# Kernel tuning notes

Hardware: AMD Instinct MI355X
Metric: run time of the kernel (lower is better)

Reference implementation:

```python
import jax, jax.numpy as jnp
import numpy as np

N = 100000      # nodes
F_IN = 512      # input features
HID = 256       # hidden
C = 50          # classes
E = 1_600_000   # edges
K = 10          # APPNP iterations
ALPHA = 1.0     # teleport prob (as hard-coded in source: APPNP(10, 1))


def setup_inputs() -> dict:
    key = jax.random.key(0)
    k1, k2, k3, k4, k5, k6 = jax.random.split(key, 6)
    x = jax.random.normal(k1, (N, F_IN), dtype=jnp.float32)
    edge_index = jax.random.randint(k2, (2, E), 0, N, dtype=jnp.int32)
    # Linear params (torch nn.Linear default init scale ~ 1/sqrt(fan_in))
    W1 = jax.random.uniform(k3, (F_IN, HID), jnp.float32, -1.0, 1.0) / np.sqrt(F_IN)
    b1 = jax.random.uniform(k4, (HID,), jnp.float32, -1.0, 1.0) / np.sqrt(F_IN)
    W2 = jax.random.uniform(k5, (HID, C), jnp.float32, -1.0, 1.0) / np.sqrt(HID)
    b2 = jax.random.uniform(k6, (C,), jnp.float32, -1.0, 1.0) / np.sqrt(HID)
    return {"x": x, "edge_index": edge_index, "W1": W1, "b1": b1, "W2": W2, "b2": b2}


def _appnp(h, edge_index):
    # gcn_norm with self-loops: A_hat = D^{-1/2} (A + I) D^{-1/2}
    loops = jnp.arange(N, dtype=edge_index.dtype)
    src = jnp.concatenate([edge_index[0], loops])  # message sources
    dst = jnp.concatenate([edge_index[1], loops])  # aggregation targets
    deg = jax.ops.segment_sum(jnp.ones_like(dst, dtype=h.dtype), dst, num_segments=N)
    dinv = jnp.where(deg > 0, jax.lax.rsqrt(deg), 0.0)
    norm = (dinv[src] * dinv[dst])[:, None]  # [E+N, 1]

    def step(z, _):
        agg = jax.ops.segment_sum(norm * z[src], dst, num_segments=N)  # [N, C]
        z = (1.0 - ALPHA) * agg + ALPHA * h
        return z, None

    z, _ = jax.lax.scan(step, h, None, length=K)
    return z


def reference(x, edge_index, W1, b1, W2, b2):
    # eval mode: dropout is identity
    h = jax.nn.relu(x @ W1 + b1)   # [N, HID]
    h = h @ W2 + b2                # [N, C]
    z = _appnp(h, edge_index)      # K-step personalized-pagerank propagation
    return jax.nn.log_softmax(z, axis=1)
```

## Files before the change

kernel.cpp:

```cpp
#include <hip/hip_runtime.h>
#include <cstdint>
#include <cstddef>

#define NROWS 100000
#define FIN 512
#define HIDDEN 256
#define NCLS 50

typedef __attribute__((ext_vector_type(8))) short s16x8;
typedef __attribute__((ext_vector_type(4))) float f32x4;

__device__ __forceinline__ unsigned short f2bf(float f) {
  unsigned int u = __float_as_uint(f);
  u += 0x7fffu + ((u >> 16) & 1u);
  return (unsigned short)(u >> 16);
}

__device__ __forceinline__ unsigned int cvt_pk_bf16(float lo, float hi) {
  unsigned int r;
  asm("v_cvt_pk_bf16_f32 %0, %1, %2" : "=v"(r) : "v"(lo), "v"(hi));
  return r;
}

__device__ __forceinline__ void gload_lds16(const void* g, void* l) {
  __builtin_amdgcn_global_load_lds(
      (const __attribute__((address_space(1))) void*)g,
      (__attribute__((address_space(3))) void*)l, 16, 0, 0);
}

__device__ __forceinline__ f32x4 mfma_bf16(s16x8 a, s16x8 b, f32x4 c) {
  return __builtin_amdgcn_mfma_f32_16x16x32_bf16(a, b, c, 0, 0, 0);
}

__global__ __launch_bounds__(256) void prep_kernel(
    const float* __restrict__ W1, const float* __restrict__ W2,
    unsigned short* __restrict__ w1t, unsigned short* __restrict__ w2t) {
  __shared__ float tile[64][65];
  const int b = blockIdx.x, t = threadIdx.x;
  if (b < 32) {
    const int k0 = (b >> 2) * 64, n0 = (b & 3) * 64;
    const int rq = t >> 6, col = t & 63;
#pragma unroll
    for (int i = 0; i < 16; ++i) {
      int row = i * 4 + rq;
      tile[row][col] = W1[(size_t)(k0 + row) * HIDDEN + n0 + col];
    }
    __syncthreads();
#pragma unroll
    for (int i = 0; i < 16; ++i) {
      int n = i * 4 + rq;
      w1t[(size_t)(n0 + n) * FIN + k0 + col] = f2bf(tile[col][n]);
    }
  } else {
    const int b2i = b - 32;
#pragma unroll
    for (int i = 0; i < 16; ++i) {
      int idx = t + i * 256;
      int c = idx >> 6;
      int k = b2i * 64 + (idx & 63);
      float v = (c < NCLS) ? W2[(size_t)k * NCLS + c] : 0.0f;
      w2t[(size_t)c * HIDDEN + k] = f2bf(v);
    }
  }
}

__global__ __launch_bounds__(512, 4) void fused_kernel(
    const float* __restrict__ x, const unsigned short* __restrict__ w1t,
    const unsigned short* __restrict__ w2t, const float* __restrict__ b1,
    const float* __restrict__ b2, float* __restrict__ out) {
  __shared__ char smem[65536];
  float* const Abase = (float*)smem;
  unsigned short* const Bbase = (unsigned short*)(smem + 32768);

  const int t = threadIdx.x;
  const int lane = t & 63, wid = t >> 6;
  const int q = lane & 15, half = lane >> 4;
  const int wr = wid >> 1, wc = wid & 1;
  const int bm = blockIdx.x;

  auto stage_A = [&](float* buf, int k0) {
#pragma unroll
    for (int i = 0; i < 2; ++i) {
      int c = t + i * 512;
      int row = c >> 3, s = c & 7;
      int grow = bm * 128 + row;
      if (grow > NROWS - 1) grow = NROWS - 1;
      gload_lds16(x + (size_t)grow * FIN + k0 + ((s ^ (row & 7)) << 2),
                  buf + c * 4);
    }
  };
  auto stage_B = [&](unsigned short* buf, int k0) {
#pragma unroll
    for (int i = 0; i < 2; ++i) {
      int c = t + i * 512;
      int col = c >> 2, s = c & 3;
      gload_lds16(w1t + (size_t)col * FIN + k0 + ((s ^ ((col >> 2) & 3)) << 3),
                  buf + c * 8);
    }
  };

  f32x4 acc[2][8];
  const f32x4 z4 = {0.f, 0.f, 0.f, 0.f};
#pragma unroll
  for (int m = 0; m < 2; ++m)
#pragma unroll
    for (int n = 0; n < 8; ++n) acc[m][n] = z4;

  auto kstep_compute = [&](int cur) {
    float* Ac = Abase + cur * 4096;
    unsigned short* Bc = Bbase + cur * 8192;
    s16x8 af[2];
#pragma unroll
    for (int m = 0; m < 2; ++m) {
      const int row = wr * 32 + m * 16 + q;
      const int cb = row * 8;
      f32x4 lo = *(const f32x4*)(Ac + (cb + ((half * 2) ^ (q & 7))) * 4);
      f32x4 hi = *(const f32x4*)(Ac + (cb + ((half * 2 + 1) ^ (q & 7))) * 4);
      union { unsigned int u[4]; s16x8 v; } cvu;
      cvu.u[0] = cvt_pk_bf16(lo[0], lo[1]);
      cvu.u[1] = cvt_pk_bf16(lo[2], lo[3]);
      cvu.u[2] = cvt_pk_bf16(hi[0], hi[1]);
      cvu.u[3] = cvt_pk_bf16(hi[2], hi[3]);
      af[m] = cvu.v;
    }
#pragma unroll
    for (int n = 0; n < 8; ++n) {
      const int col = wc * 128 + n * 16 + q;
      s16x8 bf = *(const s16x8*)(Bc + col * 32 + ((half ^ ((q >> 2) & 3)) << 3));
      acc[0][n] = mfma_bf16(af[0], bf, acc[0][n]);
      acc[1][n] = mfma_bf16(af[1], bf, acc[1][n]);
    }
  };

  stage_A(Abase, 0);
  stage_B(Bbase, 0);
  asm volatile("s_waitcnt vmcnt(0)" ::: "memory");
  __builtin_amdgcn_s_barrier();
  __builtin_amdgcn_sched_barrier(0);

  for (int ks = 0; ks < 15; ++ks) {
    const int cur = ks & 1;
    stage_A(Abase + (cur ^ 1) * 4096, (ks + 1) * 32);
    stage_B(Bbase + (cur ^ 1) * 8192, (ks + 1) * 32);
    asm volatile("s_waitcnt vmcnt(4)" ::: "memory");
    __builtin_amdgcn_s_barrier();
    __builtin_amdgcn_sched_barrier(0);
    kstep_compute(cur);
    __builtin_amdgcn_s_barrier();
    __builtin_amdgcn_sched_barrier(0);
  }
  asm volatile("s_waitcnt vmcnt(0)" ::: "memory");
  __builtin_amdgcn_s_barrier();
  __builtin_amdgcn_sched_barrier(0);
  kstep_compute(1);
  __syncthreads();

  unsigned short* const hls = (unsigned short*)smem;
  unsigned short* const wls = Bbase;
  const int p_of_wave = wid >> 2;

#pragma unroll
  for (int i = 0; i < 4; ++i) {
    int c = t + i * 512;
    int row = c >> 5, s = c & 31;
    gload_lds16(w2t + (size_t)row * HIDDEN + ((s ^ (row & 7)) << 3), wls + c * 8);
  }

  auto write_h = [&]() {
#pragma unroll
    for (int n = 0; n < 8; ++n) {
      const int col = wc * 128 + n * 16 + q;
      const float bias = b1[col];
      const int chs = col & 7;
#pragma unroll
      for (int m = 0; m < 2; ++m) {
        const int rl0 = (wr & 1) * 32 + m * 16 + half * 4;
#pragma unroll
        for (int r = 0; r < 4; ++r) {
          const int rl = rl0 + r;
          float v = fmaxf(acc[m][n][r] + bias, 0.0f);
          const int ch = (col >> 3) ^ (rl & 7);
          hls[rl * 256 + ch * 8 + chs] = f2bf(v);
        }
      }
    }
  };

  auto gemm2_pass = [&](int p) {
    f32x4 acc2[4];
#pragma unroll
    for (int n = 0; n < 4; ++n) acc2[n] = z4;
    const int arl = (wid & 3) * 16 + q;
#pragma unroll
    for (int ks = 0; ks < HIDDEN; ks += 32) {
      const int g = (ks >> 3) + half;
      s16x8 a2 = *(const s16x8*)(hls + arl * 256 + ((g ^ (arl & 7)) << 3));
#pragma unroll
      for (int n = 0; n < 4; ++n) {
        const int c = n * 16 + q;
        s16x8 b2f = *(const s16x8*)(wls + c * 256 + ((g ^ (c & 7)) << 3));
        acc2[n] = mfma_bf16(a2, b2f, acc2[n]);
      }
    }
    float bias2[4];
#pragma unroll
    for (int n = 0; n < 4; ++n) {
      const int c = n * 16 + q;
      bias2[n] = (c < NCLS) ? b2[c] : 0.0f;
    }
#pragma unroll
    for (int r = 0; r < 4; ++r) {
      float vals[4];
      float mx = -1e30f;
#pragma unroll
      for (int n = 0; n < 4; ++n) {
        const int c = n * 16 + q;
        float v = acc2[n][r] + bias2[n];
        vals[n] = v;
        if (c < NCLS) mx = fmaxf(mx, v);
      }
      for (int off = 8; off >= 1; off >>= 1)
        mx = fmaxf(mx, __shfl_xor(mx, off, 64));
      float s = 0.f;
#pragma unroll
      for (int n = 0; n < 4; ++n) {
        const int c = n * 16 + q;
        if (c < NCLS) s += __expf(vals[n] - mx);
      }
      for (int off = 8; off >= 1; off >>= 1) s += __shfl_xor(s, off, 64);
      const float lz = __logf(s);
      const int rowg = bm * 128 + p * 64 + (wid & 3) * 16 + half * 4 + r;
      if (rowg < NROWS) {
#pragma unroll
        for (int n = 0; n < 4; ++n) {
          const int c = n * 16 + q;
          if (c < NCLS) out[(size_t)rowg * NCLS + c] = vals[n] - mx - lz;
        }
      }
    }
  };

  if (p_of_wave == 0) write_h();
  __syncthreads();
  if (p_of_wave == 0) gemm2_pass(0);
  __syncthreads();
  if (p_of_wave == 1) write_h();
  __syncthreads();
  if (p_of_wave == 1) gemm2_pass(1);
}

extern "C" void kernel_launch(void* const* d_in, const int* in_sizes, int n_in,
                              void* d_out, int out_size, void* d_ws, size_t ws_size,
                              hipStream_t stream) {
  const float* x  = (const float*)d_in[0];
  const float* W1 = (const float*)d_in[2];
  const float* b1 = (const float*)d_in[3];
  const float* W2 = (const float*)d_in[4];
  const float* b2 = (const float*)d_in[5];
  float* out = (float*)d_out;

  char* ws = (char*)d_ws;
  unsigned short* w1t = (unsigned short*)(ws);
  unsigned short* w2t = (unsigned short*)(ws + 262144);

  prep_kernel<<<36, 256, 0, stream>>>(W1, W2, w1t, w2t);
  fused_kernel<<<(NROWS + 127) / 128, 512, 0, stream>>>(x, w1t, w2t, b1, b2, out);
}
```

Measured before the change: 69.27 us.

## Shrink block tile to 64 rows and stage x as bf16 via registers

Reworks the fused MLP kernel to use 256-thread blocks over 64-row tiles. fp32 x is loaded into registers, converted to bf16 once, and stored in LDS, replacing fp32 staging with a conversion on every fragment read. LDS use drops from 64KB to 40KB, and the second GEMM now reads W2 fragments directly from global memory in a single pass. The aim is higher occupancy and less LDS traffic, at the cost of more W1 re-reads per row and register-staged loads.

```diff
diff --git a/kernel.cpp b/kernel.cpp
--- a/kernel.cpp
+++ b/kernel.cpp
@@ -64,189 +64,184 @@
   }
 }
 
-__global__ __launch_bounds__(512, 4) void fused_kernel(
+__global__ __launch_bounds__(256, 4) void fused_kernel(
     const float* __restrict__ x, const unsigned short* __restrict__ w1t,
     const unsigned short* __restrict__ w2t, const float* __restrict__ b1,
     const float* __restrict__ b2, float* __restrict__ out) {
-  __shared__ char smem[65536];
-  float* const Abase = (float*)smem;
-  unsigned short* const Bbase = (unsigned short*)(smem + 32768);
+  __shared__ char smem[40960];
+  unsigned short* const Abuf = (unsigned short*)smem;
+  unsigned short* const Bbuf = (unsigned short*)(smem + 8192);
 
   const int t = threadIdx.x;
   const int lane = t & 63, wid = t >> 6;
   const int q = lane & 15, half = lane >> 4;
-  const int wr = wid >> 1, wc = wid & 1;
   const int bm = blockIdx.x;
 
-  auto stage_A = [&](float* buf, int k0) {
-#pragma unroll
-    for (int i = 0; i < 2; ++i) {
-      int c = t + i * 512;
-      int row = c >> 3, s = c & 7;
-      int grow = bm * 128 + row;
-      if (grow > NROWS - 1) grow = NROWS - 1;
-      gload_lds16(x + (size_t)grow * FIN + k0 + ((s ^ (row & 7)) << 2),
-                  buf + c * 4);
-    }
-  };
-  auto stage_B = [&](unsigned short* buf, int k0) {
-#pragma unroll
-    for (int i = 0; i < 2; ++i) {
-      int c = t + i * 512;
-      int col = c >> 2, s = c & 3;
-      gload_lds16(w1t + (size_t)col * FIN + k0 + ((s ^ ((col >> 2) & 3)) << 3),
-                  buf + c * 8);
-    }
-  };
-
-  f32x4 acc[2][8];
+  {
+    int growA = bm * 64 + (t >> 2);
+    if (growA > NROWS - 1) growA = NROWS - 1;
+  }
+  int growA = bm * 64 + (t >> 2);
+  if (growA > NROWS - 1) growA = NROWS - 1;
+  const float* const asrc = x + (size_t)growA * FIN + (t & 3) * 8;
+  unsigned short* const adst = Abuf + t * 8;
+
+  float4 rA[2][2];
+  auto load_A = [&](int slot, int k0) {
+    rA[slot][0] = *(const float4*)(asrc + k0);
+    rA[slot][1] = *(const float4*)(asrc + k0 + 4);
+  };
+  auto write_A = [&](int slot, int buf) {
+    const float4 a0 = rA[slot][0], a1 = rA[slot][1];
+    uint4 u;
+    u.x = cvt_pk_bf16(a0.x, a0.y);
+    u.y = cvt_pk_bf16(a0.z, a0.w);
+    u.z = cvt_pk_bf16(a1.x, a1.y);
+    u.w = cvt_pk_bf16(a1.z, a1.w);
+    *(uint4*)(adst + buf * 2048) = u;
+  };
+
+  const unsigned short* bsrc[4];
+  int bdst[4];
+#pragma unroll
+  for (int i = 0; i < 4; ++i) {
+    const int c = t + i * 256;
+    const int col = c >> 2, s = c & 3;
+    bsrc[i] = w1t + (size_t)col * FIN + ((s ^ ((col >> 2) & 3)) << 3);
+    bdst[i] = c * 8;
+  }
+  auto stage_B = [&](int buf, int k0) {
+#pragma unroll
+    for (int i = 0; i < 4; ++i)
+      gload_lds16(bsrc[i] + k0, Bbuf + buf * 8192 + bdst[i]);
+  };
+
+  f32x4 acc[4][4];
   const f32x4 z4 = {0.f, 0.f, 0.f, 0.f};
 #pragma unroll
-  for (int m = 0; m < 2; ++m)
-#pragma unroll
-    for (int n = 0; n < 8; ++n) acc[m][n] = z4;
-
-  auto kstep_compute = [&](int cur) {
-    float* Ac = Abase + cur * 4096;
-    unsigned short* Bc = Bbase + cur * 8192;
-    s16x8 af[2];
-#pragma unroll
-    for (int m = 0; m < 2; ++m) {
-      const int row = wr * 32 + m * 16 + q;
-      const int cb = row * 8;
-      f32x4 lo = *(const f32x4*)(Ac + (cb + ((half * 2) ^ (q & 7))) * 4);
-      f32x4 hi = *(const f32x4*)(Ac + (cb + ((half * 2 + 1) ^ (q & 7))) * 4);
-      union { unsigned int u[4]; s16x8 v; } cvu;
-      cvu.u[0] = cvt_pk_bf16(lo[0], lo[1]);
-      cvu.u[1] = cvt_pk_bf16(lo[2], lo[3]);
-      cvu.u[2] = cvt_pk_bf16(hi[0], hi[1]);
-      cvu.u[3] = cvt_pk_bf16(hi[2], hi[3]);
-      af[m] = cvu.v;
-    }
-#pragma unroll
-    for (int n = 0; n < 8; ++n) {
-      const int col = wc * 128 + n * 16 + q;
+  for (int m = 0; m < 4; ++m)
+#pragma unroll
+    for (int n = 0; n < 4; ++n) acc[m][n] = z4;
+
+  auto compute = [&](int cur) {
+    const unsigned short* Ac = Abuf + cur * 2048;
+    const unsigned short* Bc = Bbuf + cur * 8192;
+    s16x8 af[4];
+#pragma unroll
+    for (int m = 0; m < 4; ++m)
+      af[m] = *(const s16x8*)(Ac + (m * 16 + q) * 32 + half * 8);
+#pragma unroll
+    for (int n = 0; n < 4; ++n) {
+      const int col = wid * 64 + n * 16 + q;
       s16x8 bf = *(const s16x8*)(Bc + col * 32 + ((half ^ ((q >> 2) & 3)) << 3));
-      acc[0][n] = mfma_bf16(af[0], bf, acc[0][n]);
-      acc[1][n] = mfma_bf16(af[1], bf, acc[1][n]);
-    }
-  };
-
-  stage_A(Abase, 0);
-  stage_B(Bbase, 0);
+#pragma unroll
+      for (int m = 0; m < 4; ++m) acc[m][n] = mfma_bf16(af[m], bf, acc[m][n]);
+    }
+  };
+
+  stage_B(0, 0);
+  load_A(0, 0);
+  load_A(1, 32);
+  asm volatile("s_waitcnt vmcnt(2)" ::: "memory");
+  write_A(0, 0);
+
+  for (int ks = 0; ks < 15; ++ks) {
+    const int cur = ks & 1;
+    if (ks < 14) {
+      load_A(cur, (ks + 2) * 32);
+      stage_B(cur ^ 1, (ks + 1) * 32);
+      asm volatile("s_waitcnt vmcnt(6)" ::: "memory");
+    } else {
+      stage_B(cur ^ 1, (ks + 1) * 32);
+      asm volatile("s_waitcnt vmcnt(4)" ::: "memory");
+    }
+    write_A(cur ^ 1, cur ^ 1);
+    asm volatile("s_waitcnt lgkmcnt(0)" ::: "memory");
+    __builtin_amdgcn_s_barrier();
+    __builtin_amdgcn_sched_barrier(0);
+    compute(cur);
+    __builtin_amdgcn_s_barrier();
+    __builtin_amdgcn_sched_barrier(0);
+  }
   asm volatile("s_waitcnt vmcnt(0)" ::: "memory");
   __builtin_amdgcn_s_barrier();
   __builtin_amdgcn_sched_barrier(0);
-
-  for (int ks = 0; ks < 15; ++ks) {
-    const int cur = ks & 1;
-    stage_A(Abase + (cur ^ 1) * 4096, (ks + 1) * 32);
-    stage_B(Bbase + (cur ^ 1) * 8192, (ks + 1) * 32);
-    asm volatile("s_waitcnt vmcnt(4)" ::: "memory");
-    __builtin_amdgcn_s_barrier();
-    __builtin_amdgcn_sched_barrier(0);
-    kstep_compute(cur);
-    __builtin_amdgcn_s_barrier();
-    __builtin_amdgcn_sched_barrier(0);
-  }
-  asm volatile("s_waitcnt vmcnt(0)" ::: "memory");
-  __builtin_amdgcn_s_barrier();
-  __builtin_amdgcn_sched_barrier(0);
-  kstep_compute(1);
+  compute(1);
   __syncthreads();
 
-  unsigned short* const hls = (unsigned short*)smem;
-  unsigned short* const wls = Bbase;
-  const int p_of_wave = wid >> 2;
-
-#pragma unroll
-  for (int i = 0; i < 4; ++i) {
-    int c = t + i * 512;
-    int row = c >> 5, s = c & 31;
-    gload_lds16(w2t + (size_t)row * HIDDEN + ((s ^ (row & 7)) << 3), wls + c * 8);
-  }
-
-  auto write_h = [&]() {
-#pragma unroll
-    for (int n = 0; n < 8; ++n) {
-      const int col = wc * 128 + n * 16 + q;
-      const float bias = b1[col];
-      const int chs = col & 7;
-#pragma unroll
-      for (int m = 0; m < 2; ++m) {
-        const int rl0 = (wr & 1) * 32 + m * 16 + half * 4;
-#pragma unroll
-        for (int r = 0; r < 4; ++r) {
-          const int rl = rl0 + r;
-          float v = fmaxf(acc[m][n][r] + bias, 0.0f);
-          const int ch = (col >> 3) ^ (rl & 7);
-          hls[rl * 256 + ch * 8 + chs] = f2bf(v);
-        }
+  unsigned short* const hls = (unsigned short*)(smem + 8192);
+
+#pragma unroll
+  for (int n = 0; n < 4; ++n) {
+    const int col = wid * 64 + n * 16 + q;
+    const float bias = b1[col];
+    const int c3 = col >> 3, c7 = col & 7;
+#pragma unroll
+    for (int m = 0; m < 4; ++m) {
+#pragma unroll
+      for (int r = 0; r < 4; ++r) {
+        const int rl = m * 16 + half * 4 + r;
+        const int mix = (rl & 7) ^ (((rl >> 3) & 1) << 1);
+        float v = fmaxf(acc[m][n][r] + bias, 0.0f);
+        hls[rl * 256 + ((c3 ^ mix) << 3) + c7] = f2bf(v);
       }
     }
-  };
-
-  auto gemm2_pass = [&](int p) {
-    f32x4 acc2[4];
-#pragma unroll
-    for (int n = 0; n < 4; ++n) acc2[n] = z4;
-    const int arl = (wid & 3) * 16 + q;
-#pragma unroll
-    for (int ks = 0; ks < HIDDEN; ks += 32) {
-      const int g = (ks >> 3) + half;
-      s16x8 a2 = *(const s16x8*)(hls + arl * 256 + ((g ^ (arl & 7)) << 3));
+  }
+  __syncthreads();
+
+  f32x4 acc2[4];
+#pragma unroll
+  for (int n = 0; n < 4; ++n) acc2[n] = z4;
+  const int arl = wid * 16 + q;
+  const int mixa = (q & 7) ^ ((q >> 3) << 1);
+#pragma unroll
+  for (int j = 0; j < 8; ++j) {
+    const int kc = j * 4 + half;
+    s16x8 a2 = *(const s16x8*)(hls + arl * 256 + ((kc ^ mixa) << 3));
+#pragma unroll
+    for (int n = 0; n < 4; ++n) {
+      const int c = n * 16 + q;
+      s16x8 bfp = *(const s16x8*)(w2t + (size_t)c * HIDDEN + j * 32 + half * 8);
+      acc2[n] = mfma_bf16(a2, bfp, acc2[n]);
+    }
+  }
+
+  float bias2[4];
+#pragma unroll
+  for (int n = 0; n < 4; ++n) {
+    const int c = n * 16 + q;
+    bias2[n] = (c < NCLS) ? b2[c] : 0.0f;
+  }
+#pragma unroll
+  for (int r = 0; r < 4; ++r) {
+    float vals[4];
+    float mx = -1e30f;
+#pragma unroll
+    for (int n = 0; n < 4; ++n) {
+      const int c = n * 16 + q;
+      float v = acc2[n][r] + bias2[n];
+      vals[n] = v;
+      if (c < NCLS) mx = fmaxf(mx, v);
+    }
+    for (int off = 8; off >= 1; off >>= 1)
+      mx = fmaxf(mx, __shfl_xor(mx, off, 64));
+    float s = 0.f;
+#pragma unroll
+    for (int n = 0; n < 4; ++n) {
+      const int c = n * 16 + q;
+      if (c < NCLS) s += __expf(vals[n] - mx);
+    }
+    for (int off = 8; off >= 1; off >>= 1) s += __shfl_xor(s, off, 64);
+    const float lz = __logf(s);
+    const int rowg = bm * 64 + wid * 16 + half * 4 + r;
+    if (rowg < NROWS) {
 #pragma unroll
       for (int n = 0; n < 4; ++n) {
         const int c = n * 16 + q;
-        s16x8 b2f = *(const s16x8*)(wls + c * 256 + ((g ^ (c & 7)) << 3));
-        acc2[n] = mfma_bf16(a2, b2f, acc2[n]);
+        if (c < NCLS) out[(size_t)rowg * NCLS + c] = vals[n] - mx - lz;
       }
     }
-    float bias2[4];
-#pragma unroll
-    for (int n = 0; n < 4; ++n) {
-      const int c = n * 16 + q;
-      bias2[n] = (c < NCLS) ? b2[c] : 0.0f;
-    }
-#pragma unroll
-    for (int r = 0; r < 4; ++r) {
-      float vals[4];
-      float mx = -1e30f;
-#pragma unroll
-      for (int n = 0; n < 4; ++n) {
-        const int c = n * 16 + q;
-        float v = acc2[n][r] + bias2[n];
-        vals[n] = v;
-        if (c < NCLS) mx = fmaxf(mx, v);
-      }
-      for (int off = 8; off >= 1; off >>= 1)
-        mx = fmaxf(mx, __shfl_xor(mx, off, 64));
-      float s = 0.f;
-#pragma unroll
-      for (int n = 0; n < 4; ++n) {
-        const int c = n * 16 + q;
-        if (c < NCLS) s += __expf(vals[n] - mx);
-      }
-      for (int off = 8; off >= 1; off >>= 1) s += __shfl_xor(s, off, 64);
-      const float lz = __logf(s);
-      const int rowg = bm * 128 + p * 64 + (wid & 3) * 16 + half * 4 + r;
-      if (rowg < NROWS) {
-#pragma unroll
-        for (int n = 0; n < 4; ++n) {
-          const int c = n * 16 + q;
-          if (c < NCLS) out[(size_t)rowg * NCLS + c] = vals[n] - mx - lz;
-        }
-      }
-    }
-  };
-
-  if (p_of_wave == 0) write_h();
-  __syncthreads();
-  if (p_of_wave == 0) gemm2_pass(0);
-  __syncthreads();
-  if (p_of_wave == 1) write_h();
-  __syncthreads();
-  if (p_of_wave == 1) gemm2_pass(1);
+  }
 }
 
 extern "C" void kernel_launch(void* const* d_in, const int* in_sizes, int n_in,
@@ -264,5 +259,5 @@
   unsigned short* w2t = (unsigned short*)(ws + 262144);
 
   prep_kernel<<<36, 256, 0, stream>>>(W1, W2, w1t, w2t);
-  fused_kernel<<<(NROWS + 127) / 128, 512, 0, stream>>>(x, w1t, w2t, b1, b2, out);
-}
+  fused_kernel<<<(NROWS + 63) / 64, 256, 0, stream>>>(x, w1t, w2t, b1, b2, out);
+}
```

After: 84.16 us. +21.5%, slower.
